# Kernel tuning notes

Measured on AMD Instinct MI355X. Metric: run time of the kernel, lower is better.

The kernel has to match this reference:

```python
import jax, jax.numpy as jnp
import numpy as np

VOCAB = 50257
N = 2048          # neuron_dim
K = int(N * 0.01) # k-WTA winners = 20
LR = 0.01
EPS = 1e-8
T = 128           # sequence length


def setup_inputs() -> dict:
    key = jax.random.key(0)
    k1, k2, k3 = jax.random.split(key, 3)
    tokens = jax.random.randint(k1, (T,), 0, VOCAB)
    # stands in for nn.init.orthogonal_ random projection table [vocab, N]
    projection = jax.random.normal(k2, (VOCAB, N), dtype=jnp.float32)
    # sigma buffer starts at zeros in the module but is seeded by pre_train/seed_backstory;
    # use a clamped random state in [0,1) so the recurrence does real work.
    sigma = jax.random.uniform(k3, (N, N), dtype=jnp.float32)
    return {"tokens": tokens, "projection": projection, "sigma": sigma, "plasticity": 1}


def _sparse_activation(projection, tokens):
    raw = projection[tokens]                      # [T, N] gather
    top_val = jax.lax.top_k(raw, K)[0]            # [T, K]
    thr = top_val[:, -1:]                         # k-th largest value per row
    return (raw >= thr).astype(jnp.float32)       # binary k-WTA codes (ties kept, as in torch)


def reference(tokens, projection, sigma, plasticity):
    acts = _sparse_activation(projection, tokens)  # [T, N]
    x_curr = acts[:-1]                             # [T-1, N]
    x_next = acts[1:]                              # [T-1, N]
    if plasticity:
        sqrt_k = jnp.sqrt(jnp.float32(K))

        def step(sig, xs):
            x, xn = xs
            pred = sig @ x                                   # mv: [N]
            pn = jnp.linalg.norm(pred)
            overlap = jnp.dot(pred, xn) / (pn * sqrt_k + EPS)
            tension = jnp.where(pn > 0, 1.0 - overlap, 1.0)
            # Hebbian outer-product update + clamp to [0,1]
            sig = jnp.clip(sig + LR * jnp.outer(xn, x), 0.0, 1.0)
            return sig, tension

        _, tensions = jax.lax.scan(step, sigma, (x_curr, x_next))
        return tensions                                      # [T-1]
    else:
        preds = x_curr @ sigma.T                             # [T-1, N]
        dot = jnp.sum(preds * x_next, axis=-1)
        overlap = dot / (jnp.linalg.norm(preds, axis=-1) * jnp.linalg.norm(x_next, axis=-1) + EPS)
        return 1.0 - overlap
```

## Files before the change

kernel.cpp:

```cpp
#include <hip/hip_runtime.h>
#include <hip/hip_bf16.h>
#include <math.h>

#define NV    2048
#define TT    128
#define TM1   127
#define KK    20
#define LRC   0.01f
#define EPSC  1e-8f
#define CHK   20


__global__ __launch_bounds__(256) void act_kernel(
    const int* __restrict__ tokens, const float* __restrict__ proj,
    int* __restrict__ act_idx, int* __restrict__ act_cnt,
    int* __restrict__ occCnt, unsigned char* __restrict__ occList)
{
    const int t    = blockIdx.x;
    const int tid  = threadIdx.x;
    const int lane = tid & 63;
    const int wid  = tid >> 6;

    const float* __restrict__ row = proj + (size_t)tokens[t] * (size_t)NV;

    float v[8];
    #pragma unroll
    for (int r = 0; r < 8; ++r) v[r] = row[wid * 512 + r * 64 + lane];

    __shared__ float wcand[4][KK];
    __shared__ float thrS;
    __shared__ int   idxLDS[64];
    __shared__ int   cntS;

    for (int it = 0; it < KK; ++it) {
        float lm = v[0];
        #pragma unroll
        for (int r = 1; r < 8; ++r) lm = fmaxf(lm, v[r]);
        #pragma unroll
        for (int off = 1; off < 64; off <<= 1) lm = fmaxf(lm, __shfl_xor(lm, off));
        bool has = false;
        #pragma unroll
        for (int r = 0; r < 8; ++r) has = has || (v[r] == lm);
        const unsigned long long m = __ballot(has);
        if (lane == (int)(__ffsll((long long)m) - 1)) {
            bool done = false;
            #pragma unroll
            for (int r = 0; r < 8; ++r)
                if (!done && v[r] == lm) { v[r] = -__builtin_inff(); done = true; }
        }
        if (lane == 0) wcand[wid][it] = lm;
    }
    __syncthreads();

    if (tid == 0) {
        int p0 = 0, p1 = 0, p2 = 0, p3 = 0;
        float th = 0.0f;
        for (int k = 0; k < KK; ++k) {
            float bv = -__builtin_inff(); int bw = 0;
            if (p0 < KK && wcand[0][p0] > bv) { bv = wcand[0][p0]; bw = 0; }
            if (p1 < KK && wcand[1][p1] > bv) { bv = wcand[1][p1]; bw = 1; }
            if (p2 < KK && wcand[2][p2] > bv) { bv = wcand[2][p2]; bw = 2; }
            if (p3 < KK && wcand[3][p3] > bv) { bv = wcand[3][p3]; bw = 3; }
            if      (bw == 0) ++p0;
            else if (bw == 1) ++p1;
            else if (bw == 2) ++p2;
            else              ++p3;
            th = bv;
        }
        thrS = th;
    }
    __syncthreads();
    const float thr = thrS;

    if (wid == 0) {
        int base = 0;
        for (int round = 0; round < NV / 64; ++round) {
            const int i = round * 64 + lane;
            const bool p = (row[i] >= thr);
            const unsigned long long mm = __ballot(p);
            const int pos = base + (int)__popcll(mm & ((1ull << lane) - 1ull));
            if (p && pos < 64) idxLDS[pos] = i;
            base += (int)__popcll(mm);
        }
        if (lane == 0) cntS = base < 64 ? base : 64;
    }
    __syncthreads();
    const int cnt = cntS;
    if (tid == 0) act_cnt[t] = cnt;
    if (tid < cnt) {
        const int j = idxLDS[tid];
        act_idx[t * 64 + tid] = j;
        const int slot = atomicAdd(&occCnt[j], 1);
        occList[j * 128 + slot] = (unsigned char)t;
    }
}

__global__ __launch_bounds__(256) void transpose_kernel(
    const float* __restrict__ in, float* __restrict__ out)
{
    __shared__ float tile[32][33];
    const int tx = threadIdx.x;
    const int ty = threadIdx.y;
    const int x0 = blockIdx.x * 32;
    const int y0 = blockIdx.y * 32;
    #pragma unroll
    for (int k = 0; k < 4; ++k)
        tile[ty + k * 8][tx] = in[(size_t)(y0 + ty + k * 8) * NV + x0 + tx];
    __syncthreads();
    #pragma unroll
    for (int k = 0; k < 4; ++k)
        out[(size_t)(x0 + ty + k * 8) * NV + y0 + tx] = tile[tx][ty + k * 8];
}

__global__ __launch_bounds__(512) void tension_kernel(
    const float* __restrict__ sigma0, const float* __restrict__ ST0,
    const int* __restrict__ act_idx, const int* __restrict__ act_cnt,
    const int* __restrict__ occCnt, const unsigned char* __restrict__ occList,
    const int* __restrict__ plast, float* __restrict__ out)
{
    const int t    = blockIdx.x;
    const int tid  = threadIdx.x;
    const int lane = tid & 63;
    const int wid  = tid >> 6;

    __shared__ float        predS[NV];
    __shared__ unsigned int cnt32[CHK * 1024];
    __shared__ int          acur[64], anext[64];
    __shared__ float        wsum[8];

    const int ccur  = act_cnt[t];
    const int cnext = act_cnt[t + 1];
    if (tid < 64) {
        acur[tid]  = act_idx[t * 64 + tid];
        anext[tid] = act_idx[(t + 1) * 64 + tid];
    }
    __syncthreads();

    float acc[4] = {0.f, 0.f, 0.f, 0.f};
    for (int jj = 0; jj < ccur; ++jj) {
        const float* __restrict__ rowp = ST0 + (size_t)acur[jj] * NV;
        #pragma unroll
        for (int r = 0; r < 4; ++r) acc[r] += rowp[r * 512 + tid];
    }

    float dsum[4] = {0.f, 0.f, 0.f, 0.f};
    const bool plas = (plast[0] != 0);
    if (plas) {
        for (int jc = 0; jc < ccur; jc += CHK) {
            const int je = (jc + CHK < ccur) ? jc + CHK : ccur;
            for (int e = tid; e < (je - jc) * 1024; e += 512) cnt32[e] = 0u;
            __syncthreads();

            for (int jj = jc; jj < je; ++jj) {
                const int j    = acur[jj];
                const int oc   = occCnt[j];
                const int base = (jj - jc) * 1024;
                for (int p = tid; p < oc * 64; p += 512) {
                    const int o  = p >> 6;
                    const int ii = p & 63;
                    const int s  = (int)occList[j * 128 + o];
                    if (s < t) {
                        const int cs = act_cnt[s + 1];
                        if (ii < cs) {
                            const int i = act_idx[(s + 1) * 64 + ii];
                            atomicAdd(&cnt32[base + (i >> 1)],
                                      (i & 1) ? 65536u : 1u);
                        }
                    }
                }
            }
            __syncthreads();

            #pragma unroll
            for (int r = 0; r < 4; ++r) {
                const int i = r * 512 + tid;
                float ds = 0.f;
                for (int jj = jc; jj < je; ++jj) {
                    const unsigned w = cnt32[(jj - jc) * 1024 + (i >> 1)];
                    const unsigned c = (i & 1) ? (w >> 16) : (w & 0xffffu);
                    if (c) {
                        const float s0 = sigma0[(size_t)i * NV + acur[jj]];
                        ds += fminf(1.0f - s0, LRC * (float)c);
                    }
                }
                dsum[r] += ds;
            }
            __syncthreads();
        }
    }

    #pragma unroll
    for (int r = 0; r < 4; ++r) {
        const int i = r * 512 + tid;
        predS[i] = acc[r] + dsum[r];
    }
    __syncthreads();

    float loc = 0.0f;
    #pragma unroll
    for (int r = 0; r < 4; ++r) { const float p = predS[r * 512 + tid]; loc += p * p; }
    #pragma unroll
    for (int off = 32; off; off >>= 1) loc += __shfl_down(loc, off);
    if (lane == 0) wsum[wid] = loc;
    __syncthreads();

    if (tid < 64) {
        float n2 = 0.0f;
        #pragma unroll
        for (int w = 0; w < 8; ++w) n2 += wsum[w];
        float d = (tid < cnext) ? predS[anext[tid]] : 0.0f;
        #pragma unroll
        for (int off = 32; off; off >>= 1) d += __shfl_down(d, off);
        if (tid == 0) {
            const float pn = sqrtf(n2);
            float tens;
            if (plas) {
                const float overlap = d / (pn * sqrtf((float)KK) + EPSC);
                tens = (pn > 0.0f) ? (1.0f - overlap) : 1.0f;
            } else {
                const float overlap = d / (pn * sqrtf((float)cnext) + EPSC);
                tens = 1.0f - overlap;
            }
            out[t] = tens;
        }
    }
}

extern "C" void kernel_launch(void* const* d_in, const int* in_sizes, int n_in,
                              void* d_out, int out_size, void* d_ws, size_t ws_size,
                              hipStream_t stream)
{
    const int*   tokens = (const int*)d_in[0];
    const float* proj   = (const float*)d_in[1];
    const float* sigma  = (const float*)d_in[2];
    const int*   plast  = (const int*)d_in[3];
    float*       out    = (float*)d_out;

    char* ws = (char*)d_ws;
    int*           act_idx = (int*)(ws + 0);
    int*           act_cnt = (int*)(ws + 32768);
    int*           occCnt  = (int*)(ws + 33280);
    unsigned char* occList = (unsigned char*)(ws + 41472);
    float*         ST0     = (float*)(ws + 303616);

    hipMemsetAsync(occCnt, 0, NV * sizeof(int), stream);
    act_kernel<<<TT, 256, 0, stream>>>(tokens, proj, act_idx, act_cnt, occCnt, occList);
    transpose_kernel<<<dim3(NV / 32, NV / 32), dim3(32, 8), 0, stream>>>(sigma, ST0);
    tension_kernel<<<TM1, 512, 0, stream>>>(sigma, ST0, act_idx, act_cnt, occCnt,
                                            occList, plast, out);
}
```

Measured before the change: 510.1 us.

## Fuse activation and transpose kernels; reuse transposed sigma rows for Hebbian deltas

Merges the k-WTA activation kernel and the sigma transpose into one launch, using the block index to pick the role. In the tension kernel, each thread now owns four consecutive neurons and reads a float4 from each transposed sigma row. The same loaded values feed both the prediction sum and the clamped Hebbian correction, which removes the strided sigma0 column gathers. Occurrence counters shrink to 8-bit packed fields, halving shared memory, but a counter would overflow if more than 255 updates hit one element.

```diff
diff --git a/kernel.cpp b/kernel.cpp
--- a/kernel.cpp
+++ b/kernel.cpp
@@ -11,26 +11,46 @@
 #define CHK   20
 
 
-__global__ __launch_bounds__(256) void act_kernel(
+__global__ __launch_bounds__(256) void act_transpose_kernel(
     const int* __restrict__ tokens, const float* __restrict__ proj,
+    const float* __restrict__ sigma, float* __restrict__ ST0,
     int* __restrict__ act_idx, int* __restrict__ act_cnt,
     int* __restrict__ occCnt, unsigned char* __restrict__ occList)
 {
-    const int t    = blockIdx.x;
-    const int tid  = threadIdx.x;
-    const int lane = tid & 63;
-    const int wid  = tid >> 6;
-
-    const float* __restrict__ row = proj + (size_t)tokens[t] * (size_t)NV;
-
-    float v[8];
-    #pragma unroll
-    for (int r = 0; r < 8; ++r) v[r] = row[wid * 512 + r * 64 + lane];
-
+    __shared__ float tile[32][33];
     __shared__ float wcand[4][KK];
     __shared__ float thrS;
     __shared__ int   idxLDS[64];
     __shared__ int   cntS;
+
+    const int bx  = blockIdx.x;
+    const int tid = threadIdx.x;
+
+    if (bx >= TT) {
+        const int bT = bx - TT;
+        const int tx = tid & 31;
+        const int ty = tid >> 5;
+        const int x0 = (bT & 63) * 32;
+        const int y0 = (bT >> 6) * 32;
+        #pragma unroll
+        for (int k = 0; k < 4; ++k)
+            tile[ty + k * 8][tx] = sigma[(size_t)(y0 + ty + k * 8) * NV + x0 + tx];
+        __syncthreads();
+        #pragma unroll
+        for (int k = 0; k < 4; ++k)
+            ST0[(size_t)(x0 + ty + k * 8) * NV + y0 + tx] = tile[tx][ty + k * 8];
+        return;
+    }
+
+    const int t    = bx;
+    const int lane = tid & 63;
+    const int wid  = tid >> 6;
+
+    const float* __restrict__ row = proj + (size_t)tokens[t] * (size_t)NV;
+
+    float v[8];
+    #pragma unroll
+    for (int r = 0; r < 8; ++r) v[r] = row[wid * 512 + r * 64 + lane];
 
     for (int it = 0; it < KK; ++it) {
         float lm = v[0];
@@ -95,25 +115,8 @@
     }
 }
 
-__global__ __launch_bounds__(256) void transpose_kernel(
-    const float* __restrict__ in, float* __restrict__ out)
-{
-    __shared__ float tile[32][33];
-    const int tx = threadIdx.x;
-    const int ty = threadIdx.y;
-    const int x0 = blockIdx.x * 32;
-    const int y0 = blockIdx.y * 32;
-    #pragma unroll
-    for (int k = 0; k < 4; ++k)
-        tile[ty + k * 8][tx] = in[(size_t)(y0 + ty + k * 8) * NV + x0 + tx];
-    __syncthreads();
-    #pragma unroll
-    for (int k = 0; k < 4; ++k)
-        out[(size_t)(x0 + ty + k * 8) * NV + y0 + tx] = tile[tx][ty + k * 8];
-}
-
 __global__ __launch_bounds__(512) void tension_kernel(
-    const float* __restrict__ sigma0, const float* __restrict__ ST0,
+    const float* __restrict__ ST0,
     const int* __restrict__ act_idx, const int* __restrict__ act_cnt,
     const int* __restrict__ occCnt, const unsigned char* __restrict__ occList,
     const int* __restrict__ plast, float* __restrict__ out)
@@ -124,7 +127,7 @@
     const int wid  = tid >> 6;
 
     __shared__ float        predS[NV];
-    __shared__ unsigned int cnt32[CHK * 1024];
+    __shared__ unsigned int cnt8[CHK * 512];
     __shared__ int          acur[64], anext[64];
     __shared__ float        wsum[8];
 
@@ -134,27 +137,22 @@
         acur[tid]  = act_idx[t * 64 + tid];
         anext[tid] = act_idx[(t + 1) * 64 + tid];
     }
-    __syncthreads();
-
-    float acc[4] = {0.f, 0.f, 0.f, 0.f};
-    for (int jj = 0; jj < ccur; ++jj) {
-        const float* __restrict__ rowp = ST0 + (size_t)acur[jj] * NV;
-        #pragma unroll
-        for (int r = 0; r < 4; ++r) acc[r] += rowp[r * 512 + tid];
-    }
-
-    float dsum[4] = {0.f, 0.f, 0.f, 0.f};
+
     const bool plas = (plast[0] != 0);
-    if (plas) {
-        for (int jc = 0; jc < ccur; jc += CHK) {
-            const int je = (jc + CHK < ccur) ? jc + CHK : ccur;
-            for (int e = tid; e < (je - jc) * 1024; e += 512) cnt32[e] = 0u;
+
+    float accx = 0.f, accy = 0.f, accz = 0.f, accw = 0.f;
+    float dx = 0.f, dy = 0.f, dz = 0.f, dw = 0.f;
+
+    for (int jc = 0; jc < ccur; jc += CHK) {
+        const int je = (jc + CHK < ccur) ? jc + CHK : ccur;
+
+        if (plas) {
+            for (int e = tid; e < (je - jc) * 512; e += 512) cnt8[e] = 0u;
             __syncthreads();
-
             for (int jj = jc; jj < je; ++jj) {
                 const int j    = acur[jj];
                 const int oc   = occCnt[j];
-                const int base = (jj - jc) * 1024;
+                const int base = (jj - jc) * 512;
                 for (int p = tid; p < oc * 64; p += 512) {
                     const int o  = p >> 6;
                     const int ii = p & 63;
@@ -163,37 +161,40 @@
                         const int cs = act_cnt[s + 1];
                         if (ii < cs) {
                             const int i = act_idx[(s + 1) * 64 + ii];
-                            atomicAdd(&cnt32[base + (i >> 1)],
-                                      (i & 1) ? 65536u : 1u);
+                            atomicAdd(&cnt8[base + (i >> 2)],
+                                      1u << (8 * (i & 3)));
                         }
                     }
                 }
             }
-            __syncthreads();
-
-            #pragma unroll
-            for (int r = 0; r < 4; ++r) {
-                const int i = r * 512 + tid;
-                float ds = 0.f;
-                for (int jj = jc; jj < je; ++jj) {
-                    const unsigned w = cnt32[(jj - jc) * 1024 + (i >> 1)];
-                    const unsigned c = (i & 1) ? (w >> 16) : (w & 0xffffu);
-                    if (c) {
-                        const float s0 = sigma0[(size_t)i * NV + acur[jj]];
-                        ds += fminf(1.0f - s0, LRC * (float)c);
-                    }
+        }
+        __syncthreads();
+
+        for (int jj = jc; jj < je; ++jj) {
+            const float4 sv = *reinterpret_cast<const float4*>(
+                ST0 + (size_t)acur[jj] * NV + 4 * tid);
+            accx += sv.x; accy += sv.y; accz += sv.z; accw += sv.w;
+            if (plas) {
+                const unsigned w = cnt8[(jj - jc) * 512 + tid];
+                if (w) {
+                    const unsigned c0 =  w        & 255u;
+                    const unsigned c1 = (w >> 8)  & 255u;
+                    const unsigned c2 = (w >> 16) & 255u;
+                    const unsigned c3 =  w >> 24;
+                    if (c0) dx += fminf(1.0f - sv.x, LRC * (float)c0);
+                    if (c1) dy += fminf(1.0f - sv.y, LRC * (float)c1);
+                    if (c2) dz += fminf(1.0f - sv.z, LRC * (float)c2);
+                    if (c3) dw += fminf(1.0f - sv.w, LRC * (float)c3);
                 }
-                dsum[r] += ds;
             }
-            __syncthreads();
-        }
-    }
-
-    #pragma unroll
-    for (int r = 0; r < 4; ++r) {
-        const int i = r * 512 + tid;
-        predS[i] = acc[r] + dsum[r];
-    }
+        }
+        __syncthreads();
+    }
+
+    predS[4 * tid + 0] = accx + dx;
+    predS[4 * tid + 1] = accy + dy;
+    predS[4 * tid + 2] = accz + dz;
+    predS[4 * tid + 3] = accw + dw;
     __syncthreads();
 
     float loc = 0.0f;
@@ -244,8 +245,8 @@
     float*         ST0     = (float*)(ws + 303616);
 
     hipMemsetAsync(occCnt, 0, NV * sizeof(int), stream);
-    act_kernel<<<TT, 256, 0, stream>>>(tokens, proj, act_idx, act_cnt, occCnt, occList);
-    transpose_kernel<<<dim3(NV / 32, NV / 32), dim3(32, 8), 0, stream>>>(sigma, ST0);
-    tension_kernel<<<TM1, 512, 0, stream>>>(sigma, ST0, act_idx, act_cnt, occCnt,
+    act_transpose_kernel<<<TT + (NV / 32) * (NV / 32), 256, 0, stream>>>(
+        tokens, proj, sigma, ST0, act_idx, act_cnt, occCnt, occList);
+    tension_kernel<<<TM1, 512, 0, stream>>>(ST0, act_idx, act_cnt, occCnt,
                                             occList, plast, out);
 }
```

Result: faster. 494.9 us (-3.0%).
